# Kernel tuning notes

Measured on AMD Instinct MI355X. Metric: run time of the kernel, lower is better.

Reference implementation:

```python
import jax, jax.numpy as jnp
import numpy as np

THRESHOLD = 0.0
NEG_SLOPE = 0.2   # DGL GATConv leaky_relu negative slope
N, EMB, C = 4096, 2048, 10


def _gat(x, W, a_l, a_r, logm):
    """Dense masked DGL-style GATConv. x:[N,in], W:[in,H*D], a_l/a_r:[H,D],
    logm:[N,N] log edge-multiplicity (-inf where no edge). Returns [N,H,D]."""
    H, D = a_l.shape
    feat = (x @ W).reshape(-1, H, D)                      # [N,H,D]
    el = jnp.einsum('nhd,hd->nh', feat, a_l)              # per-src score
    er = jnp.einsum('nhd,hd->nh', feat, a_r)              # per-dst score
    e = jax.nn.leaky_relu(el[:, None, :] + er[None, :, :], NEG_SLOPE)  # [src,dst,H]
    logits = e + logm[:, :, None]                          # mask + self-loop multiplicity
    alpha = jax.nn.softmax(logits, axis=0)                 # edge softmax over incoming src per dst
    return jnp.einsum('sdh,she->dhe', alpha, feat)         # [N,H,D]


def setup_inputs() -> dict:
    key = jax.random.key(0)
    ks = jax.random.split(key, 12)
    s = lambda fan_in: 1.0 / np.sqrt(fan_in)
    return {
        'deep_features': jax.random.normal(ks[0], (N, EMB), jnp.float32),
        'W1':  jax.random.normal(ks[1], (2048, 1024), jnp.float32) * s(2048),
        'al1': jax.random.normal(ks[2], (1, 1024), jnp.float32) * s(1024),
        'ar1': jax.random.normal(ks[3], (1, 1024), jnp.float32) * s(1024),
        'W2':  jax.random.normal(ks[4], (1024, 2 * 512), jnp.float32) * s(1024),
        'al2': jax.random.normal(ks[5], (2, 512), jnp.float32) * s(512),
        'ar2': jax.random.normal(ks[6], (2, 512), jnp.float32) * s(512),
        'lin1_w': jax.random.normal(ks[7], (2048 + 512, 1024), jnp.float32) * s(2560),
        'lin1_b': jnp.zeros((1024,), jnp.float32),
        'c1_w': jax.random.normal(ks[8], (1024, C), jnp.float32) * s(1024),
        'c1_b': jnp.zeros((C,), jnp.float32),
        'c2_w': jax.random.normal(ks[9], (2048, C), jnp.float32) * s(2048),
        'c2_b': jnp.zeros((C,), jnp.float32),
    }


def reference(deep_features, W1, al1, ar1, W2, al2, ar2,
              lin1_w, lin1_b, c1_w, c1_b, c2_w, c2_b):
    df = deep_features                                     # [N,2048] (ResNet50 features)
    # --- build_graph: cosine similarity threshold graph on detached features ---
    dfs = jax.lax.stop_gradient(df)
    znorm = jnp.linalg.norm(dfs, axis=1, keepdims=True)
    sim = (dfs @ dfs.T) / (znorm @ znorm.T)                # symmetric cosine similarity
    n = df.shape[0]
    # adjacency from threshold (includes self since sim_ii=1>thr) + extra self-loop from dgl.add_self_loop
    mult = (sim > THRESHOLD).astype(df.dtype) + jnp.eye(n, dtype=df.dtype)
    logm = jnp.where(mult > 0, jnp.log(jnp.maximum(mult, 1e-12)), -jnp.inf)
    # --- GAT stack ---
    x = jax.nn.relu(_gat(df, W1, al1, ar1, logm).reshape(n, 1024))
    x = _gat(x, W2, al2, ar2, logm).sum(axis=1)            # sum over 2 heads -> [N,512]
    x = jnp.concatenate([df, x], axis=1)                   # [N,2560]
    x = jax.nn.leaky_relu(x @ lin1_w + lin1_b, 0.01)       # F.leaky_relu default slope
    logits1 = x @ c1_w + c1_b
    logits2 = df @ c2_w + c2_b
    return logits1, logits2
```

## Files before the change

### kernel.cpp

```cpp
#include <hip/hip_runtime.h>
#include <hip/hip_bf16.h>

typedef __hip_bfloat16 bf16;
typedef __attribute__((ext_vector_type(8))) short short8;
typedef __attribute__((ext_vector_type(4))) float f32x4;

#define NN 4096
#define L2E 1.4426950408889634f

__device__ inline float br_sum(float v, float* sd){
  #pragma unroll
  for(int s=32; s>0; s>>=1) v += __shfl_down(v, s, 64);
  int t = threadIdx.x;
  if ((t & 63) == 0) sd[t >> 6] = v;
  __syncthreads();
  float r = (sd[0] + sd[1]) + (sd[2] + sd[3]);
  __syncthreads();
  return r;
}

__device__ inline void gl2lds(const bf16* g, unsigned int* lds){
  __builtin_amdgcn_global_load_lds(
      (const __attribute__((address_space(1))) unsigned int*)g,
      (__attribute__((address_space(3))) unsigned int*)lds, 16, 0, 0);
}

template<int N> __device__ inline void waitvm(){
  if constexpr (N==0)       asm volatile("s_waitcnt vmcnt(0)" ::: "memory");
  else if constexpr (N==4)  asm volatile("s_waitcnt vmcnt(4)" ::: "memory");
  else if constexpr (N==6)  asm volatile("s_waitcnt vmcnt(6)" ::: "memory");
  else if constexpr (N==8)  asm volatile("s_waitcnt vmcnt(8)" ::: "memory");
  else if constexpr (N==12) asm volatile("s_waitcnt vmcnt(12)" ::: "memory");
  else if constexpr (N==18) asm volatile("s_waitcnt vmcnt(18)" ::: "memory");
  else if constexpr (N==24) asm volatile("s_waitcnt vmcnt(24)" ::: "memory");
}
__device__ inline void pipe_barrier(){
  __builtin_amdgcn_s_barrier();
  asm volatile("" ::: "memory");
}

__global__ __launch_bounds__(256)
void prep_all_k(const float* __restrict__ df, const float* __restrict__ W1,
                const float* __restrict__ W2, const float* __restrict__ lw,
                bf16* __restrict__ dfb, bf16* __restrict__ W1tb,
                bf16* __restrict__ W2tb, bf16* __restrict__ lwcat,
                const float* __restrict__ c2w, const float* __restrict__ c2b,
                float* __restrict__ out2,
                const float* __restrict__ c1b, float* __restrict__ out1,
                float* __restrict__ SA, float* __restrict__ SB2)
{
  int b = blockIdx.x, t = threadIdx.x;
  if (b < 4096){
    __shared__ float sd4[4];
    int n = b, k0 = t*8;
    size_t i = (size_t)n*2048 + k0;
    f32x4 v0 = *(const f32x4*)(df + i);
    f32x4 v1 = *(const f32x4*)(df + i + 4);
    short8 s;
    float acc[10] = {};
    #pragma unroll
    for(int q=0;q<4;q++){
      bf16 h0 = __float2bfloat16(v0[q]);
      bf16 h1 = __float2bfloat16(v1[q]);
      s[q]   = *(short*)&h0;
      s[4+q] = *(short*)&h1;
      #pragma unroll
      for(int c=0;c<10;c++){
        acc[c] += v0[q]*c2w[(k0+q)*10 + c] + v1[q]*c2w[(k0+4+q)*10 + c];
      }
    }
    *(short8*)(dfb + i) = s;
    #pragma unroll
    for(int c=0;c<10;c++){
      float r = br_sum(acc[c], sd4);
      if(t==0) out2[n*10 + c] = r + c2b[c];
    }
    return;
  }
  if (b >= 5504){
    int r = (b - 5504)*256 + t;
    #pragma unroll
    for(int c=0;c<10;c++) out1[r*10 + c] = c1b[c];
    SA[r] = 0.f; SA[r + 4096] = 0.f;
    #pragma unroll
    for(int q=0;q<4;q++) SB2[r + q*4096] = 0.f;
    return;
  }
  b -= 4096;
  const float* src; bf16* dst; int rb, cb, dstld; bool dup=false;
  if (b < 512){            src=W1; dst=W1tb;  rb=(b>>4)<<6; cb=(b&15)<<6; dstld=2048; }
  else if (b < 768){ b-=512; src=W2; dst=W2tb; rb=(b>>4)<<6; cb=(b&15)<<6; dstld=1024; }
  else { b-=768; src=lw; dst=lwcat; rb=(b>>4)<<6; cb=(b&15)<<6; dstld=3072; dup=(rb>=2048); }
  __shared__ bf16 tile[64][65];
  #pragma unroll
  for(int i=0;i<16;i++){
    int lin=i*256+t, tr=lin>>6, tc=lin&63;
    tile[tr][tc] = __float2bfloat16(src[(size_t)(rb+tr)*1024 + cb+tc]);
  }
  __syncthreads();
  #pragma unroll
  for(int i=0;i<16;i++){
    int lin=i*256+t, tc=lin>>6, tr=lin&63;
    bf16 v = tile[tr][tc];
    dst[(size_t)(cb+tc)*dstld + rb+tr] = v;
    if(dup) dst[(size_t)(cb+tc)*dstld + rb+tr + 512] = v;
  }
}

__device__ __forceinline__
void adj_body(const bf16* __restrict__ A, unsigned int* __restrict__ Cm,
              unsigned int* SH, int idx)
{
  unsigned int* As = SH;
  unsigned int* Bs = SH + 6144;
  const int tid = threadIdx.x;
  int by = (int)((65.0f - sqrtf(4225.0f - 8.0f*(float)idx)) * 0.5f);
  while ((by+1)*(65-(by+1))/2 <= idx) by++;
  while (by*(65-by)/2 > idx) by--;
  int bx = by + (idx - by*(65-by)/2);
  const int bm = by*128, bn = bx*128;
  const int lane = tid&63, wid = tid>>6;
  const int wr = (wid>>1)*64, wc = (wid&1)*64;
  const int quad = lane>>4, mr = lane&15;
  const int L4 = lane>>2;
  const int lsw = (lane&3) ^ ((lane>>3)&3);
  const int qsw4 = ((quad ^ ((mr>>1)&3)) << 2);

  f32x4 acc[4][4];
  #pragma unroll
  for(int i=0;i<4;i++)
    #pragma unroll
    for(int j=0;j<4;j++) acc[i][j] = (f32x4){0.f,0.f,0.f,0.f};

  auto stage = [&](int kb, int p){
    #pragma unroll
    for(int c2=0; c2<2; c2++){
      int row = (wid*2+c2)*16 + L4;
      gl2lds(A + (size_t)(bm+row)*2048 + kb + lsw*8, &As[p*2048 + (wid*2+c2)*256]);
      gl2lds(A + (size_t)(bn+row)*2048 + kb + lsw*8, &Bs[p*2048 + (wid*2+c2)*256]);
    }
  };
  auto compute = [&](int p){
    short8 af[4], bfr[4];
    #pragma unroll
    for(int i=0;i<4;i++)  af[i]  = *(const short8*)&As[p*2048 + (wr + i*16 + mr)*16 + qsw4];
    #pragma unroll
    for(int j=0;j<4;j++)  bfr[j] = *(const short8*)&Bs[p*2048 + (wc + j*16 + mr)*16 + qsw4];
    #pragma unroll
    for(int i=0;i<4;i++)
      #pragma unroll
      for(int j=0;j<4;j++)
        acc[i][j] = __builtin_amdgcn_mfma_f32_16x16x32_bf16(af[i], bfr[j], acc[i][j], 0,0,0);
  };

  stage(0,0); stage(32,1);
  int p = 0;
  #pragma unroll 1
  for(int it=0; it<63; it++){
    waitvm<4>();
    pipe_barrier();
    if (it+2 < 64) stage(32*(it+2), p==0?2:p-1);
    compute(p);
    p = (p==2)?0:p+1;
  }
  waitvm<0>();
  pipe_barrier();
  compute(p);

  #pragma unroll
  for(int i=0;i<4;i++){
    #pragma unroll
    for(int j=0;j<4;j++){
      int cbase = bn + wc + j*16;
      unsigned long long b[4];
      #pragma unroll
      for(int reg=0; reg<4; reg++){
        float v = acc[i][j][reg];
        unsigned long long msk = __ballot(v > 0.f);
        b[reg] = msk;
        if (mr == 0){
          int r = bm + wr + i*16 + quad*4 + reg;
          unsigned int x = (unsigned int)(msk >> (quad*16)) & 0xFFFFu;
          x = (x | (x << 8)) & 0x00FF00FFu;
          x = (x | (x << 4)) & 0x0F0F0F0Fu;
          x = (x | (x << 2)) & 0x33333333u;
          x = (x | (x << 1)) & 0x55555555u;
          if (r >= cbase && r < cbase + 16) x += 1u << (2*(r - cbase));
          Cm[(size_t)r*256 + (cbase>>4)] = x;
        }
      }
      if (bx > by){
        unsigned int x = 0;
        #pragma unroll
        for(int reg=0; reg<4; reg++){
          unsigned long long t = (b[reg] >> mr) & 0x0001000100010001ULL;
          unsigned int f = (unsigned int)((t | (t>>15) | (t>>30) | (t>>45)) & 0xFULL);
          x |= ((f&1u) | ((f&2u)<<7) | ((f&4u)<<14) | ((f&8u)<<21)) << (2*reg);
        }
        if (quad == 0){
          int c = cbase + mr;
          Cm[(size_t)c*256 + ((bm + wr + i*16)>>4)] = x;
        }
      }
    }
  }
}

template<int EPI, int TN, int DUALA, int K, int LDA, int LDBT, int LDC,
         int K1, int LDA2, int WT, int NS, int EL>
__device__ __forceinline__
void gemm_body(const bf16* __restrict__ Ag, const bf16* __restrict__ Bt,
               void* __restrict__ Cv, const float* __restrict__ bias,
               const bf16* __restrict__ Ag2, bf16* __restrict__ Ct,
               const float* __restrict__ eA, const float* __restrict__ eB,
               float* __restrict__ eX, float* __restrict__ eY,
               unsigned int* SH, int bid)
{
  constexpr int NJ  = TN/32;
  constexpr int D   = 2 + TN/64;
  constexpr int NIT = K/32;
  unsigned int* As = SH;
  unsigned int* Bs = SH + NS*2048;
  const int tid = threadIdx.x;
  const int by = 4*(bid&7) + ((bid>>3)&3);
  const int bx = bid>>5;
  const int bm = by*128, bn = bx*TN;
  const int lane = tid&63, wid = tid>>6;
  const int wr = (wid>>1)*64, wc = (wid&1)*(TN/2);
  const int quad = lane>>4, mr = lane&15;
  const int L4 = lane>>2;
  const int lsw = (lane&3) ^ ((lane>>3)&3);
  const int qsw4 = ((quad ^ ((mr>>1)&3)) << 2);

  f32x4 acc[4][NJ];
  #pragma unroll
  for(int i=0;i<4;i++)
    #pragma unroll
    for(int j=0;j<NJ;j++) acc[i][j] = (f32x4){0.f,0.f,0.f,0.f};

  auto stage = [&](int kb, int p){
    #pragma unroll
    for(int c2=0; c2<2; c2++){
      int row = (wid*2+c2)*16 + L4;
      const bf16* ap;
      if (DUALA && kb >= K1) ap = Ag2 + (size_t)(bm+row)*LDA2 + (kb-K1);
      else                   ap = Ag  + (size_t)(bm+row)*LDA  + kb;
      gl2lds(ap + lsw*8, &As[p*2048 + (wid*2+c2)*256]);
    }
    #pragma unroll
    for(int c2=0; c2<TN/64; c2++){
      int row = (wid*(TN/64)+c2)*16 + L4;
      gl2lds(Bt + (size_t)(bn+row)*LDBT + kb + lsw*8,
             &Bs[p*(TN*16) + (wid*(TN/64)+c2)*256]);
    }
  };
  auto compute = [&](int p){
    short8 af[4], bfr[NJ];
    #pragma unroll
    for(int i=0;i<4;i++)
      af[i]  = *(const short8*)&As[p*2048 + (wr + i*16 + mr)*16 + qsw4];
    #pragma unroll
    for(int j=0;j<NJ;j++)
      bfr[j] = *(const short8*)&Bs[p*(TN*16) + (wc + j*16 + mr)*16 + qsw4];
    #pragma unroll
    for(int i=0;i<4;i++)
      #pragma unroll
      for(int j=0;j<NJ;j++)
        acc[i][j] = __builtin_amdgcn_mfma_f32_16x16x32_bf16(af[i], bfr[j], acc[i][j], 0,0,0);
  };

  #pragma unroll
  for(int s=0; s<NS-1; s++) stage(32*s, s);
  int p = 0;
  #pragma unroll 1
  for(int it=0; it<NIT-(NS-1); it++){
    waitvm<(NS-2)*D>();
    pipe_barrier();
    stage(32*(it+NS-1), (p+NS-1)&(NS-1));
    compute(p); p=(p+1)&(NS-1);
  }
  waitvm<0>(); pipe_barrier();
  #pragma unroll 1
  for(int r=0; r<NS-1; r++){ compute(p); p=(p+1)&(NS-1); }

  if (EPI==1 || EPI==2 || EPI==4){
    #pragma unroll
    for(int i=0;i<4;i++){
      #pragma unroll
      for(int j=0;j<NJ;j++){
        #pragma unroll
        for(int reg=0; reg<4; reg++){
          int r = bm + wr + i*16 + quad*4 + reg;
          int c = bn + wc + j*16 + mr;
          float v = acc[i][j][reg];
          if (EPI==1){ ((bf16*)Cv)[(size_t)r*LDC + c] = __float2bfloat16(fmaxf(v,0.f)); }
          if (EPI==2){ ((bf16*)Cv)[(size_t)r*LDC + c] = __float2bfloat16(v); }
          if (EPI==4){ float w = v + bias[c];
                       ((float*)Cv)[(size_t)r*LDC + c] = w > 0.f ? w : 0.01f*w; }
        }
      }
    }
  }

  if (EPI==5){
    #pragma unroll
    for(int i=0;i<4;i++){
      #pragma unroll
      for(int reg=0; reg<4; reg++){
        float lg[10];
        #pragma unroll
        for(int cl=0;cl<10;cl++) lg[cl] = 0.f;
        #pragma unroll
        for(int j=0;j<NJ;j++){
          int c = bn + wc + j*16 + mr;
          float w = acc[i][j][reg] + bias[c];
          w = w > 0.f ? w : 0.01f*w;
          #pragma unroll
          for(int cl=0;cl<10;cl++) lg[cl] += w * eA[c*10 + cl];
        }
        #pragma unroll
        for(int s=1;s<16;s<<=1)
          #pragma unroll
          for(int cl=0;cl<10;cl++) lg[cl] += __shfl_xor(lg[cl], s);
        if (mr == 0){
          int n = bm + wr + i*16 + quad*4 + reg;
          #pragma unroll
          for(int cl=0;cl<10;cl++) atomicAdd(&eX[n*10 + cl], lg[cl]);
        }
      }
    }
  }

  if (EL){
    float* elp = eX; float* erp = eY;
    if (EL==2){ int hh = bn >> 9; elp += hh*NN; erp += hh*NN; }
    #pragma unroll
    for(int i=0;i<4;i++){
      #pragma unroll
      for(int reg=0; reg<4; reg++){
        float pl = 0.f, pr = 0.f;
        #pragma unroll
        for(int j=0;j<NJ;j++){
          int c = bn + wc + j*16 + mr;
          float v = acc[i][j][reg];
          pl += v * eA[c];
          pr += v * eB[c];
        }
        #pragma unroll
        for(int s=1;s<16;s<<=1){ pl += __shfl_xor(pl, s); pr += __shfl_xor(pr, s); }
        if (mr == 0){
          int n = bm + wr + i*16 + quad*4 + reg;
          atomicAdd(&elp[n], pl*L2E);
          atomicAdd(&erp[n], pr*L2E);
        }
      }
    }
  }

  if (WT){
    __syncthreads();
    bf16* T = (bf16*)SH;
    #pragma unroll
    for(int i=0;i<4;i++)
      #pragma unroll
      for(int j=0;j<NJ;j++)
        #pragma unroll
        for(int reg=0; reg<4; reg++){
          int rl = wr + i*16 + quad*4 + reg;
          int cl = wc + j*16 + mr;
          T[rl*66 + cl] = __float2bfloat16(acc[i][j][reg]);
        }
    __syncthreads();
    #pragma unroll
    for(int w=0; w<TN/4; w++){
      int cl = wid*(TN/4) + w;
      unsigned int v = (unsigned int)(*(unsigned short*)&T[(2*lane)*66 + cl]) |
                       ((unsigned int)(*(unsigned short*)&T[(2*lane+1)*66 + cl]) << 16);
      *(unsigned int*)&Ct[(size_t)(bn+cl)*4096 + bm + 2*lane] = v;
    }
  }
}

template<int EPI, int TN, int DUALA, int K, int LDA, int LDBT, int LDC,
         int K1, int LDA2, int WT, int NS, int EL>
__global__ __launch_bounds__(256)
void gemm_k(const bf16* __restrict__ Ag, const bf16* __restrict__ Bt,
            void* __restrict__ Cv, const float* __restrict__ bias,
            const bf16* __restrict__ Ag2, bf16* __restrict__ Ct,
            const float* __restrict__ eA, const float* __restrict__ eB,
            float* __restrict__ eX, float* __restrict__ eY)
{
  __shared__ unsigned int SH[NS*2048 + NS*TN*16];
  gemm_body<EPI,TN,DUALA,K,LDA,LDBT,LDC,K1,LDA2,WT,NS,EL>(
      Ag, Bt, Cv, bias, Ag2, Ct, eA, eB, eX, eY, SH, blockIdx.x);
}

__global__ __launch_bounds__(256)
void agg2_k(const bf16* __restrict__ P, const bf16* __restrict__ P2,
            const bf16* __restrict__ featT, bf16* __restrict__ x2cat)
{
  __shared__ unsigned int SH[8*2048 + 8*128*16];
  int b = blockIdx.x;
  const bf16* A = (b < 128) ? P : P2;
  const bf16* B = (b < 128) ? featT : featT + (size_t)512*4096;
  bf16* C = (b < 128) ? x2cat : x2cat + 512;
  gemm_body<2,128,0,4096,4096,4096,1024,0,0,0,8,0>(
      A, B, C, nullptr, nullptr, nullptr, nullptr, nullptr, nullptr, nullptr,
      SH, b & 127);
}

__global__ __launch_bounds__(256)
void adjfeat_k(const bf16* __restrict__ dfb, unsigned int* __restrict__ mult2,
               const bf16* __restrict__ W1tb, bf16* __restrict__ featT,
               const float* __restrict__ al1, const float* __restrict__ ar1,
               float* __restrict__ el1, float* __restrict__ er1)
{
  __shared__ unsigned int SH[12288];
  int b = blockIdx.x;
  if (b < 528){
    adj_body(dfb, mult2, SH, b);
  } else {
    gemm_body<0,64,0,2048,2048,2048,1024,0,0,1,4,1>(
        dfb, W1tb, nullptr, nullptr, nullptr, featT, al1, ar1, el1, er1,
        SH, b-528);
  }
}

__global__ __launch_bounds__(256)
void colp_k(const float* __restrict__ el, const float* __restrict__ er,
            const unsigned int* __restrict__ mult2,
            float* __restrict__ cm, float* __restrict__ cinv,
            bf16* __restrict__ P, bf16* __restrict__ P2)
{
  __shared__ float sd[256];
  int d = blockIdx.x & 4095, hs = blockIdx.x >> 12, t = threadIdx.x;
  el += hs*NN; er += hs*NN; cm += hs*NN; cinv += hs*NN;
  float erd = er[d];
  unsigned int bits = mult2[(size_t)d*256 + t];
  float tv[16];
  float mx = -1e30f;
  const float* ep = el + t*16;
  #pragma unroll
  for(int h=0; h<4; h++){
    f32x4 ev = *(const f32x4*)(ep + h*4);
    #pragma unroll
    for(int q2=0;q2<4;q2++){
      int q = h*4 + q2;
      unsigned int mu = (bits >> (2*q)) & 3u;
      float x = ev[q2] + erd;
      x = fmaxf(x, 0.2f*x);
      if (mu == 2u) x += 1.0f;
      tv[q] = mu ? x : -1e30f;
      mx = fmaxf(mx, tv[q]);
    }
  }
  #pragma unroll
  for(int s=32; s>0; s>>=1) mx = fmaxf(mx, __shfl_down(mx, s, 64));
  if ((t & 63) == 0) sd[t >> 6] = mx;
  __syncthreads();
  float M = fmaxf(fmaxf(sd[0], sd[1]), fmaxf(sd[2], sd[3]));
  __syncthreads();
  float sum = 0.f;
  #pragma unroll
  for(int q=0;q<16;q++) sum += (tv[q] > -1e29f) ? __builtin_exp2f(tv[q]-M) : 0.f;
  sum = br_sum(sum, sd);
  if(t==0){ cm[d] = M; cinv[d] = 1.f/sum; }
  bf16* Pd = (hs == 0) ? P : P2;
  if (Pd){
    float inv = 1.f/sum;
    unsigned int pk[8];
    #pragma unroll
    for(int h=0; h<4; h++){
      #pragma unroll
      for(int q2=0; q2<4; q2++){
        int q = h*4+q2;
        float v = (tv[q] > -1e29f) ? __builtin_exp2f(tv[q]-M)*inv : 0.f;
        bf16 hb = __float2bfloat16(v);
        unsigned short us = *(unsigned short*)&hb;
        if (q2 & 1) pk[h*2 + (q2>>1)] |= ((unsigned int)us << 16);
        else        pk[h*2 + (q2>>1)]  = (unsigned int)us;
      }
    }
    uint4* dst = (uint4*)(Pd + (size_t)d*4096 + t*16);
    dst[0] = *(uint4*)&pk[0];
    dst[1] = *(uint4*)&pk[4];
  }
}

__global__ __launch_bounds__(256)
void pbuild_k(const float* __restrict__ el, const float* __restrict__ er,
              const float* __restrict__ cm, const float* __restrict__ cinv,
              const unsigned int* __restrict__ mult2, bf16* __restrict__ P)
{
  int d = blockIdx.x, t = threadIdx.x;
  const float erd = er[d], md = cm[d], invd = cinv[d];
  unsigned int bits = mult2[(size_t)d*256 + t];
  unsigned int pk[8];
  const float* ep = el + t*16;
  #pragma unroll
  for(int h=0; h<4; h++){
    f32x4 ev = *(const f32x4*)(ep + h*4);
    #pragma unroll
    for(int q2=0; q2<4; q2++){
      int q = h*4+q2;
      unsigned int mu = (bits >> (2*q)) & 3u;
      float x = ev[q2] + erd;
      x = fmaxf(x, 0.2f*x);
      float v = __builtin_exp2f(x + (mu>1u ? 1.0f : 0.0f) - md) * invd;
      v = mu ? v : 0.0f;
      bf16 hb = __float2bfloat16(v);
      unsigned short us = *(unsigned short*)&hb;
      if (q2 & 1) pk[h*2 + (q2>>1)] |= ((unsigned int)us << 16);
      else        pk[h*2 + (q2>>1)]  = (unsigned int)us;
    }
  }
  uint4* dst = (uint4*)(P + (size_t)d*4096 + t*16);
  dst[0] = *(uint4*)&pk[0];
  dst[1] = *(uint4*)&pk[4];
}

extern "C" void kernel_launch(void* const* d_in, const int* in_sizes, int n_in,
                              void* d_out, int out_size, void* d_ws, size_t ws_size,
                              hipStream_t stream) {
  (void)in_sizes; (void)n_in; (void)out_size;
  const float* df  = (const float*)d_in[0];
  const float* W1  = (const float*)d_in[1];
  const float* al1 = (const float*)d_in[2];
  const float* ar1 = (const float*)d_in[3];
  const float* W2  = (const float*)d_in[4];
  const float* al2 = (const float*)d_in[5];
  const float* ar2 = (const float*)d_in[6];
  const float* lw  = (const float*)d_in[7];
  const float* lb  = (const float*)d_in[8];
  const float* c1w = (const float*)d_in[9];
  const float* c1b = (const float*)d_in[10];
  const float* c2w = (const float*)d_in[11];
  const float* c2b = (const float*)d_in[12];
  float* out = (float*)d_out;

  char* Wp = (char*)d_ws;
  bf16* W1tb  = (bf16*)(Wp);
  bf16* W2tb  = (bf16*)(Wp + ( 4u<<20));
  bf16* lwcat = (bf16*)(Wp + ( 6u<<20));
  unsigned int* mult2 = (unsigned int*)(Wp + (12u<<20));
  bf16* dfb   = (bf16*)(Wp + (16u<<20));
  float* SB2  = (float*)(Wp + (32u<<20));
  bf16* featT = (bf16*)(Wp + (40u<<20));
  float* SA   = (float*)(Wp + (48u<<20));
  bf16* x1b   = (bf16*)(Wp + (48u<<20));
  bf16* x2cat = (bf16*)(Wp + (48u<<20));
  bf16* P     = (bf16*)(Wp + (56u<<20));
  bf16* P2    = (bf16*)(Wp + (88u<<20));
  const bool bigws = ws_size >= ((size_t)120 << 20);
  float *el1 = SA,        *er1 = SA + 4096;
  float *m1  = SA + 8192, *i1  = SA + 12288;
  float *el2 = SB2,           *er2 = SB2 + 8192;
  float *m2  = SB2 + 16384,   *i2  = SB2 + 24576;

  prep_all_k<<<5520,256,0,stream>>>(df, W1, W2, lw, dfb, W1tb, W2tb, lwcat,
                                    c2w, c2b, out + NN*10, c1b, out, SA, SB2);

  adjfeat_k<<<1040,256,0,stream>>>(dfb, mult2, W1tb, featT, al1, ar1, el1, er1);

  colp_k<<<4096,256,0,stream>>>(el1, er1, mult2, m1, i1, P, nullptr);

  gemm_k<1,128,0,4096,4096,4096,1024,0,0,0,8,0><<<256,256,0,stream>>>(
      P, featT, x1b, nullptr, nullptr, nullptr, nullptr, nullptr, nullptr, nullptr);

  gemm_k<0,128,0,1024,1024,1024,1024,0,0,1,4,2><<<256,256,0,stream>>>(
      x1b, W2tb, nullptr, nullptr, nullptr, featT, al2, ar2, el2, er2);

  colp_k<<<8192,256,0,stream>>>(el2, er2, mult2, m2, i2, P, bigws ? P2 : nullptr);

  if (bigws){
    agg2_k<<<256,256,0,stream>>>(P, P2, featT, x2cat);
  } else {
    gemm_k<2,64,0,4096,4096,4096,1024,0,0,0,8,0><<<256,256,0,stream>>>(
        P, featT, x2cat, nullptr, nullptr, nullptr, nullptr, nullptr, nullptr, nullptr);
    pbuild_k<<<4096,256,0,stream>>>(el2+NN, er2+NN, m2+NN, i2+NN, mult2, P);
    gemm_k<2,64,0,4096,4096,4096,1024,0,0,0,8,0><<<256,256,0,stream>>>(
        P, featT + (size_t)512*4096, x2cat + 512, nullptr, nullptr, nullptr,
        nullptr, nullptr, nullptr, nullptr);
  }

  gemm_k<5,128,1,3072,2048,3072,1024,2048,1024,0,8,0><<<256,256,0,stream>>>(
      dfb, lwcat, nullptr, lb, x2cat, nullptr, c1w, nullptr, out, nullptr);
}
```

Before: 488.6 us.

## Unfuse classifier from final GEMM and cut pipeline stages from 8 to 4

The final lin1 GEMM no longer computes the 10-class classifier in its epilogue with per-row atomics. It now writes the leaky-ReLU fp32 activations to a workspace buffer, and a new per-row kernel computes logits1. All 4096-K aggregation GEMMs and the final GEMM also drop from 8 to 4 LDS pipeline stages, which shrinks shared memory and may raise occupancy but hides less memory latency. The workspace layout is shifted to make room for x3. This removes atomic contention and the heavy epilogue register pressure, at the cost of an extra launch and a 16MB round trip through memory.

```diff
diff --git a/kernel.cpp b/kernel.cpp
--- a/kernel.cpp
+++ b/kernel.cpp
@@ -46,7 +46,6 @@
                 bf16* __restrict__ W2tb, bf16* __restrict__ lwcat,
                 const float* __restrict__ c2w, const float* __restrict__ c2b,
                 float* __restrict__ out2,
-                const float* __restrict__ c1b, float* __restrict__ out1,
                 float* __restrict__ SA, float* __restrict__ SB2)
 {
   int b = blockIdx.x, t = threadIdx.x;
@@ -79,8 +78,6 @@
   }
   if (b >= 5504){
     int r = (b - 5504)*256 + t;
-    #pragma unroll
-    for(int c=0;c<10;c++) out1[r*10 + c] = c1b[c];
     SA[r] = 0.f; SA[r + 4096] = 0.f;
     #pragma unroll
     for(int q=0;q<4;q++) SB2[r + q*4096] = 0.f;
@@ -302,35 +299,6 @@
     }
   }
 
-  if (EPI==5){
-    #pragma unroll
-    for(int i=0;i<4;i++){
-      #pragma unroll
-      for(int reg=0; reg<4; reg++){
-        float lg[10];
-        #pragma unroll
-        for(int cl=0;cl<10;cl++) lg[cl] = 0.f;
-        #pragma unroll
-        for(int j=0;j<NJ;j++){
-          int c = bn + wc + j*16 + mr;
-          float w = acc[i][j][reg] + bias[c];
-          w = w > 0.f ? w : 0.01f*w;
-          #pragma unroll
-          for(int cl=0;cl<10;cl++) lg[cl] += w * eA[c*10 + cl];
-        }
-        #pragma unroll
-        for(int s=1;s<16;s<<=1)
-          #pragma unroll
-          for(int cl=0;cl<10;cl++) lg[cl] += __shfl_xor(lg[cl], s);
-        if (mr == 0){
-          int n = bm + wr + i*16 + quad*4 + reg;
-          #pragma unroll
-          for(int cl=0;cl<10;cl++) atomicAdd(&eX[n*10 + cl], lg[cl]);
-        }
-      }
-    }
-  }
-
   if (EL){
     float* elp = eX; float* erp = eY;
     if (EL==2){ int hh = bn >> 9; elp += hh*NN; erp += hh*NN; }
@@ -399,12 +367,12 @@
 void agg2_k(const bf16* __restrict__ P, const bf16* __restrict__ P2,
             const bf16* __restrict__ featT, bf16* __restrict__ x2cat)
 {
-  __shared__ unsigned int SH[8*2048 + 8*128*16];
+  __shared__ unsigned int SH[4*2048 + 4*128*16];
   int b = blockIdx.x;
   const bf16* A = (b < 128) ? P : P2;
   const bf16* B = (b < 128) ? featT : featT + (size_t)512*4096;
   bf16* C = (b < 128) ? x2cat : x2cat + 512;
-  gemm_body<2,128,0,4096,4096,4096,1024,0,0,0,8,0>(
+  gemm_body<2,128,0,4096,4096,4096,1024,0,0,0,4,0>(
       A, B, C, nullptr, nullptr, nullptr, nullptr, nullptr, nullptr, nullptr,
       SH, b & 127);
 }
@@ -517,6 +485,25 @@
   uint4* dst = (uint4*)(P + (size_t)d*4096 + t*16);
   dst[0] = *(uint4*)&pk[0];
   dst[1] = *(uint4*)&pk[4];
+}
+
+__global__ __launch_bounds__(256)
+void cls2_k(const float* __restrict__ x3, const float* __restrict__ c1w,
+            const float* __restrict__ c1b, float* __restrict__ out)
+{
+  __shared__ float sd[256];
+  int n = blockIdx.x, t = threadIdx.x, k0 = t*4;
+  f32x4 xv = *(const f32x4*)(x3 + (size_t)n*1024 + k0);
+  float acc[10] = {};
+  #pragma unroll
+  for(int q=0;q<4;q++){
+    #pragma unroll
+    for(int c=0;c<10;c++) acc[c] += xv[q] * c1w[(k0+q)*10 + c];
+  }
+  for(int c=0;c<10;c++){
+    float r = br_sum(acc[c], sd);
+    if(t==0) out[n*10 + c] = r + c1b[c];
+  }
 }
 
 extern "C" void kernel_launch(void* const* d_in, const int* in_sizes, int n_in,
@@ -545,26 +532,27 @@
   unsigned int* mult2 = (unsigned int*)(Wp + (12u<<20));
   bf16* dfb   = (bf16*)(Wp + (16u<<20));
   float* SB2  = (float*)(Wp + (32u<<20));
-  bf16* featT = (bf16*)(Wp + (40u<<20));
-  float* SA   = (float*)(Wp + (48u<<20));
-  bf16* x1b   = (bf16*)(Wp + (48u<<20));
-  bf16* x2cat = (bf16*)(Wp + (48u<<20));
-  bf16* P     = (bf16*)(Wp + (56u<<20));
-  bf16* P2    = (bf16*)(Wp + (88u<<20));
-  const bool bigws = ws_size >= ((size_t)120 << 20);
+  float* x3   = (float*)(Wp + (32u<<20));
+  bf16* featT = (bf16*)(Wp + (48u<<20));
+  float* SA   = (float*)(Wp + (56u<<20));
+  bf16* x1b   = (bf16*)(Wp + (56u<<20));
+  bf16* x2cat = (bf16*)(Wp + (56u<<20));
+  bf16* P     = (bf16*)(Wp + (64u<<20));
+  bf16* P2    = (bf16*)(Wp + (96u<<20));
+  const bool bigws = ws_size >= ((size_t)128 << 20);
   float *el1 = SA,        *er1 = SA + 4096;
   float *m1  = SA + 8192, *i1  = SA + 12288;
   float *el2 = SB2,           *er2 = SB2 + 8192;
   float *m2  = SB2 + 16384,   *i2  = SB2 + 24576;
 
   prep_all_k<<<5520,256,0,stream>>>(df, W1, W2, lw, dfb, W1tb, W2tb, lwcat,
-                                    c2w, c2b, out + NN*10, c1b, out, SA, SB2);
+                                    c2w, c2b, out + NN*10, SA, SB2);
 
   adjfeat_k<<<1040,256,0,stream>>>(dfb, mult2, W1tb, featT, al1, ar1, el1, er1);
 
   colp_k<<<4096,256,0,stream>>>(el1, er1, mult2, m1, i1, P, nullptr);
 
-  gemm_k<1,128,0,4096,4096,4096,1024,0,0,0,8,0><<<256,256,0,stream>>>(
+  gemm_k<1,128,0,4096,4096,4096,1024,0,0,0,4,0><<<256,256,0,stream>>>(
       P, featT, x1b, nullptr, nullptr, nullptr, nullptr, nullptr, nullptr, nullptr);
 
   gemm_k<0,128,0,1024,1024,1024,1024,0,0,1,4,2><<<256,256,0,stream>>>(
@@ -575,14 +563,16 @@
   if (bigws){
     agg2_k<<<256,256,0,stream>>>(P, P2, featT, x2cat);
   } else {
-    gemm_k<2,64,0,4096,4096,4096,1024,0,0,0,8,0><<<256,256,0,stream>>>(
+    gemm_k<2,64,0,4096,4096,4096,1024,0,0,0,4,0><<<256,256,0,stream>>>(
         P, featT, x2cat, nullptr, nullptr, nullptr, nullptr, nullptr, nullptr, nullptr);
     pbuild_k<<<4096,256,0,stream>>>(el2+NN, er2+NN, m2+NN, i2+NN, mult2, P);
-    gemm_k<2,64,0,4096,4096,4096,1024,0,0,0,8,0><<<256,256,0,stream>>>(
+    gemm_k<2,64,0,4096,4096,4096,1024,0,0,0,4,0><<<256,256,0,stream>>>(
         P, featT + (size_t)512*4096, x2cat + 512, nullptr, nullptr, nullptr,
         nullptr, nullptr, nullptr, nullptr);
   }
 
-  gemm_k<5,128,1,3072,2048,3072,1024,2048,1024,0,8,0><<<256,256,0,stream>>>(
-      dfb, lwcat, nullptr, lb, x2cat, nullptr, c1w, nullptr, out, nullptr);
-}
+  gemm_k<4,128,1,3072,2048,3072,1024,2048,1024,0,4,0><<<256,256,0,stream>>>(
+      dfb, lwcat, x3, lb, x2cat, nullptr, nullptr, nullptr, nullptr, nullptr);
+
+  cls2_k<<<4096,256,0,stream>>>(x3, c1w, c1b, out);
+}
```

After: 437.5 us. 10.5% less time.
